# Kernel tuning notes

Hardware: AMD Instinct MI355X
Metric: run time of the kernel (lower is better)

The kernel has to match this reference:

```python
import jax, jax.numpy as jnp
import numpy as np

EPS = 1e-12

def _l2norm(x):
    return x * jax.lax.rsqrt(jnp.maximum(jnp.sum(x * x, -1, keepdims=True), EPS))

def _reverse_seq(x, lens):
    # per-row reversal of the first `lens[b]` steps (tf.reverse_sequence semantics)
    T = x.shape[1]
    ar = jnp.arange(T)[None, :]
    idx = jnp.where(ar < lens[:, None], lens[:, None] - 1 - ar, ar)
    return jnp.take_along_axis(x, idx[:, :, None], axis=1)

def _lstm(x, lens, Wx, Wh, b):
    # x: [B,T,D]; outputs zeroed past lens, state frozen past lens (dynamic_rnn)
    B, T, _ = x.shape
    H = Wh.shape[0]
    xW = jnp.einsum('btd,dh->bth', x, Wx) + b  # [B,T,4H]
    def step(carry, inp):
        h, c = carry
        xw_t, t = inp
        gates = xw_t + h @ Wh
        i, f, g, o = jnp.split(gates, 4, axis=-1)
        c_new = jax.nn.sigmoid(f) * c + jax.nn.sigmoid(i) * jnp.tanh(g)
        h_new = jax.nn.sigmoid(o) * jnp.tanh(c_new)
        valid = (t < lens)[:, None]
        return (jnp.where(valid, h_new, h), jnp.where(valid, c_new, c)), jnp.where(valid, h_new, 0.0)
    z = jnp.zeros((B, H), x.dtype)
    _, outs = jax.lax.scan(step, (z, z), (xW.transpose(1, 0, 2), jnp.arange(T)))
    return outs.transpose(1, 0, 2)

def _bilstm(x, lens, Wx_f, Wh_f, b_f, Wx_b, Wh_b, b_b):
    fwd = _lstm(x, lens, Wx_f, Wh_f, b_f)
    bwd = _reverse_seq(_lstm(_reverse_seq(x, lens), lens, Wx_b, Wh_b, b_b), lens)
    return jnp.concatenate([fwd, bwd], -1)  # [B,T,2R]

def setup_inputs() -> dict:
    B, T, CTX, D, R, HA, TD = 4096, 80, 10, 300, 200, 100, 256
    V, NTOK, NTY, PL = 100000, 250, 113, 3
    ks = jax.random.split(jax.random.key(0), 16)
    f32 = jnp.float32
    return {
        'input_data': jax.random.randint(ks[0], (B, T), 0, V, jnp.int32),
        'entMentIndex': jax.random.randint(ks[1], (B, 5), 0, B * T, jnp.int32),
        'entCtxLeftIndex': jax.random.randint(ks[2], (B, CTX), 0, B * T, jnp.int32),
        'entCtxRightIndex': jax.random.randint(ks[3], (B, CTX), 0, B * T, jnp.int32),
        'entMentLent': jnp.full((B, 1), 5.0, f32),
        'ctxLeftLent': jnp.full((B, 1), float(CTX), f32),
        'ctxRightLent': jnp.full((B, 1), float(CTX), f32),
        'type_path': jax.random.randint(ks[4], (NTY, PL), 0, NTOK, jnp.int32),
        'word_embed': jax.random.normal(ks[5], (V, D), f32) * 0.1,
        'h_m': jax.random.normal(ks[6], (D, HA), f32) * 0.01,
        'h1': jax.random.normal(ks[7], (2 * R, HA), f32) * 0.01,
        'h2': jax.random.normal(ks[8], (HA, 1), f32) * 0.01,
        'Wx_f': jax.random.normal(ks[9], (D, 4 * R), f32) * 0.05,
        'Wh_f': jax.random.normal(ks[10], (R, 4 * R), f32) * 0.05,
        'b_f': jnp.zeros((4 * R,), f32),
        'Wx_b': jax.random.normal(ks[11], (D, 4 * R), f32) * 0.05,
        'Wh_b': jax.random.normal(ks[12], (R, 4 * R), f32) * 0.05,
        'b_b': jnp.zeros((4 * R,), f32),
        'dense_W': jax.random.normal(ks[13], (D + 2 * R, TD), f32) * 0.05,
        'dense_b': jnp.zeros((TD,), f32),
        'type_tok': jax.random.normal(ks[14], (NTOK, TD), f32) * 0.01,
    }

def reference(input_data, entMentIndex, entCtxLeftIndex, entCtxRightIndex,
              entMentLent, ctxLeftLent, ctxRightLent, type_path, word_embed,
              h_m, h1, h2, Wx_f, Wh_f, b_f, Wx_b, Wh_b, b_b,
              dense_W, dense_b, type_tok):
    D = word_embed.shape[1]
    # flattened sentence embeddings with zero padding row at the end
    flat = jnp.concatenate(
        [jnp.take(word_embed, input_data.reshape(-1), axis=0),
         jnp.zeros((1, D), word_embed.dtype)], 0)
    # mention feature: mean of mention word vectors
    f1 = jnp.take(flat, entMentIndex, axis=0).sum(1) / entMentLent  # [B,D]
    # context features via shared BiLSTM
    left = jnp.take(flat, entCtxLeftIndex, axis=0)
    right = jnp.take(flat, entCtxRightIndex, axis=0)
    f2 = _bilstm(left, ctxLeftLent[:, 0].astype(jnp.int32), Wx_f, Wh_f, b_f, Wx_b, Wh_b, b_b)
    f3 = _bilstm(right, ctxRightLent[:, 0].astype(jnp.int32), Wx_f, Wh_f, b_f, Wx_b, Wh_b, b_b)
    ctx = jnp.concatenate([f2, f3], 1)  # [B, 2*CTX, 2R]
    # attention pooling (non-BBN branch uses relu)
    att = jax.nn.relu(jnp.einsum('btr,rh->bth', ctx, h1) + (f1 @ h_m)[:, None, :])
    w = jax.nn.softmax((att @ h2)[:, :, 0], axis=-1)  # [B, 2*CTX]
    ctx_feat = jnp.einsum('btr,bt->br', ctx, w)
    feat = jnp.concatenate([f1, ctx_feat], 1)  # [B, D+2R]
    ent = _l2norm(jax.nn.relu(feat @ dense_W + dense_b))  # [B, TD]
    # type-path embeddings: sum token embeddings along path, l2-normalize
    type_pad = jnp.concatenate([type_tok, jnp.zeros((1, type_tok.shape[1]), type_tok.dtype)], 0)
    type_norm = _l2norm(jnp.take(type_pad, type_path, axis=0).sum(1))  # [NTY, TD]
    return ent @ type_norm.T  # [B, NTY]
```

## Files before the change

kernel.cpp:

```cpp
#include <hip/hip_runtime.h>
#include <hip/hip_bf16.h>

constexpr int B    = 4096;
constexpr int T    = 80;
constexpr int CTXN = 10;
constexpr int D    = 300;
constexpr int R    = 200;
constexpr int HA   = 100;
constexpr int TD   = 256;
constexpr int NTY  = 113;
constexpr int PL   = 3;
constexpr int NTOK = 250;
constexpr int CTX2 = 20;
constexpr int R2   = 400;
constexpr int FEAT = 700;

constexpr int XSB  = 320;
constexpr int KH   = 256;
constexpr int KW   = 576;
constexpr int NB   = 832;
constexpr int CTXS = 448;
constexpr int F1S  = 320;
constexpr int FBS  = 704;
constexpr int FMS  = 128;
constexpr int MX   = 2 * B * CTXN;

typedef __attribute__((ext_vector_type(8))) short bf16x8;
typedef __attribute__((ext_vector_type(4))) float f32x4;

__device__ __forceinline__ ushort f2bf(float f) {
    union { float f; uint32_t u; } x{f};
    uint32_t r = x.u + 0x7fff + ((x.u >> 16) & 1);
    return (ushort)(r >> 16);
}
__device__ __forceinline__ float bf2f(ushort u) {
    union { uint32_t u; float f; } x{(uint32_t)u << 16};
    return x.f;
}

#define GLD_LDS(g, l) __builtin_amdgcn_global_load_lds( \
    (const __attribute__((address_space(1))) void*)(g), \
    (__attribute__((address_space(3))) void*)(l), 16, 0, 0)

constexpr int NWC = 2 * NB * KW;
__global__ void k_prepw3(const float* __restrict__ Wx_f, const float* __restrict__ Wh_f,
                         const float* __restrict__ bf_, const float* __restrict__ Wx_b,
                         const float* __restrict__ Wh_b, const float* __restrict__ bb_,
                         ushort* __restrict__ Wcat, float* __restrict__ biasb) {
    int gid = blockIdx.x * blockDim.x + threadIdx.x;
    if (gid < NWC) {
        int k = gid % KW;
        int q = gid / KW;
        int np = q % NB, dir = q / NB;
        int rb = np >> 6, g = (np >> 4) & 3, ri = np & 15;
        int r = rb * 16 + ri, col = g * 200 + r;
        float v = 0.f;
        if (r < R) {
            if (k < KH) {
                if (k < R) v = (dir ? Wh_b : Wh_f)[(size_t)k * 800 + col];
            } else {
                int kx = k - KH;
                if (kx < D) v = (dir ? Wx_b : Wx_f)[(size_t)kx * 800 + col];
            }
        }
        Wcat[gid] = f2bf(v);
    } else if (gid < NWC + 2 * NB) {
        int t = gid - NWC;
        int np = t % NB, dirb = t / NB;
        int rb = np >> 6, g = (np >> 4) & 3, ri = np & 15;
        int r = rb * 16 + ri, col = g * 200 + r;
        biasb[t] = (r < R) ? (dirb ? bb_ : bf_)[col] : 0.f;
    }
}

__global__ void k_preph1(const float* __restrict__ h1, ushort* __restrict__ h1t) {
    int gid = blockIdx.x * blockDim.x + threadIdx.x;
    if (gid >= FMS * CTXS) return;
    int k = gid % CTXS, n = gid / CTXS;
    float v = (n < HA && k < R2) ? h1[(size_t)k * HA + n] : 0.f;
    h1t[gid] = f2bf(v);
}
__global__ void k_prephm(const float* __restrict__ h_m, ushort* __restrict__ h_mt) {
    int gid = blockIdx.x * blockDim.x + threadIdx.x;
    if (gid >= FMS * F1S) return;
    int k = gid % F1S, n = gid / F1S;
    float v = (n < HA && k < D) ? h_m[(size_t)k * HA + n] : 0.f;
    h_mt[gid] = f2bf(v);
}
__global__ void k_prepdw(const float* __restrict__ dW, ushort* __restrict__ dWt) {
    int gid = blockIdx.x * blockDim.x + threadIdx.x;
    if (gid >= TD * FBS) return;
    int k = gid % FBS, n = gid / FBS;
    float v = (k < FEAT) ? dW[(size_t)k * TD + n] : 0.f;
    dWt[gid] = f2bf(v);
}

__global__ void k_gatherb(const int* __restrict__ idxL, const int* __restrict__ idxR,
                          const int* __restrict__ input_data,
                          const float* __restrict__ we,
                          ushort* __restrict__ xb) {
    int row = blockIdx.x * 4 + (threadIdx.x >> 6);
    int lane = threadIdx.x & 63;
    if (row >= MX) return;
    int side = row / (B * CTXN);
    int bt = row % (B * CTXN);
    int idx = (side ? idxR : idxL)[bt];
    int w = (idx >= 0 && idx < B * T) ? input_data[idx] : -1;
    ushort* dst = xb + (size_t)row * XSB;
    if (lane < XSB / 8) {
        int e0 = lane * 8;
        ushort tmp[8];
        #pragma unroll
        for (int j = 0; j < 8; ++j) {
            int e = e0 + j;
            float f = (w >= 0 && e < D) ? we[(size_t)w * D + e] : 0.f;
            tmp[j] = f2bf(f);
        }
        *reinterpret_cast<bf16x8*>(dst + e0) = *reinterpret_cast<bf16x8*>(tmp);
    }
}

__global__ void k_f1(const int* __restrict__ ment_idx,
                     const float* __restrict__ ment_lent,
                     const int* __restrict__ input_data,
                     const float* __restrict__ we,
                     ushort* __restrict__ featb, ushort* __restrict__ f1b) {
    int b = blockIdx.x;
    __shared__ int wrow[5];
    if (threadIdx.x < 5) {
        int idx = ment_idx[b * 5 + threadIdx.x];
        wrow[threadIdx.x] = (idx >= 0 && idx < B * T) ? input_data[idx] : -1;
    }
    __syncthreads();
    float inv = 1.0f / ment_lent[b];
    for (int d = threadIdx.x; d < F1S; d += blockDim.x) {
        float s = 0.f;
        if (d < D) {
            #pragma unroll
            for (int j = 0; j < 5; ++j) {
                int w = wrow[j];
                if (w >= 0) s += we[(size_t)w * D + d];
            }
            s *= inv;
        }
        ushort u = f2bf(s);
        if (d < D) featb[(size_t)b * FBS + d] = u;
        f1b[(size_t)b * F1S + d] = u;
    }
}

template<int MODE>
__global__ __launch_bounds__(256) void k_mfma(
    const ushort* __restrict__ A, int lda,
    const ushort* __restrict__ Bt, int ldb,
    float* __restrict__ C, int ldc, int K,
    const float* __restrict__ aux) {
    __shared__ __align__(16) ushort As[128 * 64];
    __shared__ __align__(16) ushort Bs[64 * 64];
    int tid = threadIdx.x, wave = tid >> 6, lane = tid & 63;
    int m0 = blockIdx.y * 128, n0 = blockIdx.x * 64;
    int wr = wave >> 1, wc = wave & 1;
    f32x4 acc[4][2] = {};

    for (int k0 = 0; k0 < K; k0 += 64) {
        #pragma unroll
        for (int p = 0; p < 4; ++p) {
            int chunk = p * 4 + wave;
            int row = chunk * 8 + (lane >> 3);
            int ss = (lane & 7) ^ (row & 7);
            GLD_LDS(A + (size_t)(m0 + row) * lda + k0 + ss * 8, As + chunk * 512);
        }
        #pragma unroll
        for (int p = 0; p < 2; ++p) {
            int chunk = p * 4 + wave;
            int row = chunk * 8 + (lane >> 3);
            int ss = (lane & 7) ^ (row & 7);
            GLD_LDS(Bt + (size_t)(n0 + row) * ldb + k0 + ss * 8, Bs + chunk * 512);
        }
        __syncthreads();
        #pragma unroll
        for (int kk = 0; kk < 2; ++kk) {
            bf16x8 a[4], bf[2];
            #pragma unroll
            for (int m = 0; m < 4; ++m) {
                int r = wr * 64 + m * 16 + (lane & 15);
                int ss = (kk * 4 + (lane >> 4)) ^ (r & 7);
                a[m] = *(const bf16x8*)&As[r * 64 + ss * 8];
            }
            #pragma unroll
            for (int n = 0; n < 2; ++n) {
                int r = wc * 32 + n * 16 + (lane & 15);
                int ss = (kk * 4 + (lane >> 4)) ^ (r & 7);
                bf[n] = *(const bf16x8*)&Bs[r * 64 + ss * 8];
            }
            #pragma unroll
            for (int m = 0; m < 4; ++m)
                #pragma unroll
                for (int n = 0; n < 2; ++n)
                    acc[m][n] = __builtin_amdgcn_mfma_f32_16x16x32_bf16(a[m], bf[n], acc[m][n], 0, 0, 0);
        }
        __syncthreads();
    }
    #pragma unroll
    for (int m = 0; m < 4; ++m) {
        #pragma unroll
        for (int n = 0; n < 2; ++n) {
            int c = n0 + wc * 32 + n * 16 + (lane & 15);
            #pragma unroll
            for (int j = 0; j < 4; ++j) {
                int rr = m0 + wr * 64 + m * 16 + (lane >> 4) * 4 + j;
                float v = acc[m][n][j];
                if (MODE == 1) v = fmaxf(v + aux[c], 0.f);
                C[(size_t)rr * ldc + c] = v;
            }
        }
    }
}

__global__ __launch_bounds__(512, 1) void k_lstm(
    const ushort* __restrict__ xb,
    const ushort* __restrict__ Wcat,
    const float* __restrict__ biasb,
    const float* __restrict__ lentL, const float* __restrict__ lentR,
    ushort* __restrict__ ctxb) {
    __shared__ __align__(16) ushort hS[64 * 256];
    __shared__ __align__(16) ushort xS[64 * 320];
    __shared__ __align__(16) ushort wS[8][2][2048];
    __shared__ int lenS[64];
    __shared__ int xrowS[CTXN][64];

    const int tid = threadIdx.x, wave = tid >> 6, lane = tid & 63;
    const int z = blockIdx.x >> 6, rg = blockIdx.x & 63;
    const int side = z >> 1, dir = z & 1;
    const int b0 = rg * 64;
    const ushort* Wd = Wcat + (size_t)dir * NB * KW;
    const int rl = lane & 15, ch = lane >> 4;

    if (tid < 64) {
        int b = b0 + tid;
        int len = (int)((side ? lentR : lentL)[b]);
        len = min(max(len, 0), CTXN);
        lenS[tid] = len;
        for (int s = 0; s < CTXN; ++s) {
            int tt = dir ? ((s < len) ? (len - 1 - s) : s) : s;
            xrowS[s][tid] = (side * (B * CTXN) + b * CTXN + tt) * XSB;
        }
    }
    {
        uint4 zz{0, 0, 0, 0};
        for (int i = tid; i < 64 * 256 / 8; i += 512)
            reinterpret_cast<uint4*>(hS)[i] = zz;
    }
    {
        bf16x8 zz{};
        int ng = dir ? 31 : 25;
        int coff = dir ? R : 0;
        for (int i = tid; i < 640 * ng; i += 512) {
            int bt = i / ng, gix = i - bt * ng;
            int row = bt / CTXN, t = bt - row * CTXN;
            *reinterpret_cast<bf16x8*>(
                ctxb + ((size_t)(b0 + row) * CTX2 + side * CTXN + t) * CTXS + coff + gix * 8) = zz;
        }
    }

    const int nrb = (wave + 8 < 13) ? 2 : 1;
    float bias_[2][4];
    #pragma unroll
    for (int g = 0; g < 4; ++g) {
        bias_[0][g] = biasb[dir * NB + wave * 64 + g * 16 + rl];
        bias_[1][g] = (nrb > 1) ? biasb[dir * NB + (wave + 8) * 64 + g * 16 + rl] : 0.f;
    }
    float cst[2][16];
    #pragma unroll
    for (int i = 0; i < 2; ++i)
        #pragma unroll
        for (int j = 0; j < 16; ++j) cst[i][j] = 0.f;

    __syncthreads();

    #pragma unroll
    for (int i = 0; i < 5; ++i) {
        int chunk = wave * 5 + i;
        int p = chunk * 64 + lane;
        int row = p / 40, c8s = p - row * 40;
        int c8 = c8s ^ (row & 7);
        GLD_LDS(xb + xrowS[0][row] + c8 * 8, xS + chunk * 512);
    }
    __syncthreads();

    float hnew[2][16];

    for (int s = 0; s < CTXN; ++s) {
        const int kstart = (s == 0) ? KH : 0;
        #pragma unroll
        for (int rbi = 0; rbi < 2; ++rbi) {
            if (rbi < nrb) {
                const int rb = rbi ? (wave + 8) : wave;
                const ushort* wb = Wd + (size_t)rb * 64 * KW;
                const int nit = (KW - kstart) >> 5;
                f32x4 acc[4][4];
                #pragma unroll
                for (int m = 0; m < 4; ++m)
                    #pragma unroll
                    for (int g = 0; g < 4; ++g) acc[m][g] = f32x4{0.f, 0.f, 0.f, 0.f};

                #pragma unroll
                for (int i = 0; i < 4; ++i) {
                    int p = i * 64 + lane;
                    int n = p >> 2, c8s = p & 3;
                    int c8 = c8s ^ ((n >> 1) & 3);
                    GLD_LDS(wb + (size_t)n * KW + kstart + c8 * 8, &wS[wave][0][0] + i * 512);
                }
                for (int t = 0; t < nit; ++t) {
                    int k0 = kstart + t * 32;
                    if (t + 1 < nit) {
                        int k1 = k0 + 32;
                        ushort* dst = &wS[wave][(t + 1) & 1][0];
                        #pragma unroll
                        for (int i = 0; i < 4; ++i) {
                            int p = i * 64 + lane;
                            int n = p >> 2, c8s = p & 3;
                            int c8 = c8s ^ ((n >> 1) & 3);
                            GLD_LDS(wb + (size_t)n * KW + k1 + c8 * 8, dst + i * 512);
                        }
                        asm volatile("s_waitcnt vmcnt(4)" ::: "memory");
                    } else {
                        asm volatile("s_waitcnt vmcnt(0)" ::: "memory");
                    }
                    const ushort* abase; int astr, kof;
                    if (k0 < KH) { abase = hS; astr = 256; kof = k0 >> 3; }
                    else         { abase = xS; astr = 320; kof = (k0 - KH) >> 3; }
                    bf16x8 af[4];
                    #pragma unroll
                    for (int m = 0; m < 4; ++m) {
                        int row = m * 16 + rl;
                        int g = (kof + ch) ^ (row & 7);
                        af[m] = *reinterpret_cast<const bf16x8*>(&abase[row * astr + g * 8]);
                    }
                    const ushort* wbuf = &wS[wave][t & 1][0];
                    bf16x8 bfr[4];
                    #pragma unroll
                    for (int g4 = 0; g4 < 4; ++g4) {
                        int col = g4 * 16 + rl;
                        int c8 = ch ^ ((rl >> 1) & 3);
                        bfr[g4] = *reinterpret_cast<const bf16x8*>(&wbuf[col * 32 + c8 * 8]);
                    }
                    #pragma unroll
                    for (int m = 0; m < 4; ++m)
                        #pragma unroll
                        for (int g4 = 0; g4 < 4; ++g4)
                            acc[m][g4] = __builtin_amdgcn_mfma_f32_16x16x32_bf16(
                                af[m], bfr[g4], acc[m][g4], 0, 0, 0);
                }
                #pragma unroll
                for (int m = 0; m < 4; ++m) {
                    #pragma unroll
                    for (int j = 0; j < 4; ++j) {
                        int row = m * 16 + ch * 4 + j;
                        float gi = acc[m][0][j] + bias_[rbi][0];
                        float gf = acc[m][1][j] + bias_[rbi][1];
                        float gg = acc[m][2][j] + bias_[rbi][2];
                        float go = acc[m][3][j] + bias_[rbi][3];
                        float si = 1.f / (1.f + __expf(-gi));
                        float sf = 1.f / (1.f + __expf(-gf));
                        float so = 1.f / (1.f + __expf(-go));
                        float cn = sf * cst[rbi][m * 4 + j] + si * tanhf(gg);
                        float hn = so * tanhf(cn);
                        if (s < lenS[row]) cst[rbi][m * 4 + j] = cn;
                        hnew[rbi][m * 4 + j] = hn;
                    }
                }
            }
        }
        __syncthreads();
        #pragma unroll
        for (int rbi = 0; rbi < 2; ++rbi) {
            if (rbi < nrb) {
                const int rb = rbi ? (wave + 8) : wave;
                const int r = rb * 16 + rl;
                if (r < R) {
                    #pragma unroll
                    for (int m = 0; m < 4; ++m) {
                        #pragma unroll
                        for (int j = 0; j < 4; ++j) {
                            int row = m * 16 + ch * 4 + j;
                            int len = lenS[row];
                            if (s < len) {
                                ushort hv = f2bf(hnew[rbi][m * 4 + j]);
                                hS[row * 256 + (((r >> 3) ^ (row & 7)) << 3) + (r & 7)] = hv;
                                int tpos = dir ? (len - 1 - s) : s;
                                ctxb[((size_t)(b0 + row) * CTX2 + side * CTXN + tpos) * CTXS
                                     + dir * R + r] = hv;
                            }
                        }
                    }
                }
            }
        }
        if (s + 1 < CTXN) {
            #pragma unroll
            for (int i = 0; i < 5; ++i) {
                int chunk = wave * 5 + i;
                int p = chunk * 64 + lane;
                int row = p / 40, c8s = p - row * 40;
                int c8 = c8s ^ (row & 7);
                GLD_LDS(xb + xrowS[s + 1][row] + c8 * 8, xS + chunk * 512);
            }
        }
        __syncthreads();
    }
}

__global__ __launch_bounds__(256) void k_attsc(
    const ushort* __restrict__ ctxb, const ushort* __restrict__ h1t,
    const float* __restrict__ fm, const float* __restrict__ h2,
    float* __restrict__ scores) {
    __shared__ __align__(16) ushort As[128 * 64];
    __shared__ __align__(16) ushort Bs[128 * 64];
    __shared__ float sred[128][2];
    __shared__ float h2s[128];
    int tid = threadIdx.x, wave = tid >> 6, lane = tid & 63;
    int m0 = blockIdx.x * 128;
    if (tid < 128) h2s[tid] = (tid < HA) ? h2[tid] : 0.f;
    int wr = wave >> 1, wc = wave & 1;
    f32x4 acc[4][4] = {};

    for (int k0 = 0; k0 < CTXS; k0 += 64) {
        #pragma unroll
        for (int p = 0; p < 4; ++p) {
            int chunk = p * 4 + wave;
            int row = chunk * 8 + (lane >> 3);
            int ss = (lane & 7) ^ (row & 7);
            GLD_LDS(ctxb + (size_t)(m0 + row) * CTXS + k0 + ss * 8, As + chunk * 512);
        }
        #pragma unroll
        for (int p = 0; p < 4; ++p) {
            int chunk = p * 4 + wave;
            int row = chunk * 8 + (lane >> 3);
            int ss = (lane & 7) ^ (row & 7);
            GLD_LDS(h1t + (size_t)row * CTXS + k0 + ss * 8, Bs + chunk * 512);
        }
        __syncthreads();
        #pragma unroll
        for (int kk = 0; kk < 2; ++kk) {
            bf16x8 a[4], bf[4];
            #pragma unroll
            for (int m = 0; m < 4; ++m) {
                int r = wr * 64 + m * 16 + (lane & 15);
                int ss = (kk * 4 + (lane >> 4)) ^ (r & 7);
                a[m] = *(const bf16x8*)&As[r * 64 + ss * 8];
            }
            #pragma unroll
            for (int n = 0; n < 4; ++n) {
                int r = wc * 64 + n * 16 + (lane & 15);
                int ss = (kk * 4 + (lane >> 4)) ^ (r & 7);
                bf[n] = *(const bf16x8*)&Bs[r * 64 + ss * 8];
            }
            #pragma unroll
            for (int m = 0; m < 4; ++m)
                #pragma unroll
                for (int n = 0; n < 4; ++n)
                    acc[m][n] = __builtin_amdgcn_mfma_f32_16x16x32_bf16(a[m], bf[n], acc[m][n], 0, 0, 0);
        }
        __syncthreads();
    }
    #pragma unroll
    for (int m = 0; m < 4; ++m) {
        #pragma unroll
        for (int j = 0; j < 4; ++j) {
            int rl = wr * 64 + m * 16 + (lane >> 4) * 4 + j;
            int brow = (m0 + rl) / CTX2;
            float v = 0.f;
            #pragma unroll
            for (int n = 0; n < 4; ++n) {
                int c = wc * 64 + n * 16 + (lane & 15);
                float a = acc[m][n][j] + fm[(size_t)brow * FMS + c];
                v += fmaxf(a, 0.f) * h2s[c];
            }
            #pragma unroll
            for (int o = 1; o < 16; o <<= 1) v += __shfl_xor(v, o, 64);
            if ((lane & 15) == 0) sred[rl][wc] = v;
        }
    }
    __syncthreads();
    if (tid < 128) scores[m0 + tid] = sred[tid][0] + sred[tid][1];
}

__global__ void k_att2(const float* __restrict__ scores,
                       const ushort* __restrict__ ctxb,
                       ushort* __restrict__ featb) {
    int b = blockIdx.x;
    float sc[CTX2];
    #pragma unroll
    for (int t = 0; t < CTX2; ++t) sc[t] = scores[b * CTX2 + t];
    float mx = -1e30f;
    #pragma unroll
    for (int t = 0; t < CTX2; ++t) mx = fmaxf(mx, sc[t]);
    float w[CTX2], sum = 0.f;
    #pragma unroll
    for (int t = 0; t < CTX2; ++t) { w[t] = __expf(sc[t] - mx); sum += w[t]; }
    float inv = 1.f / sum;
    for (int col = threadIdx.x; col < R2; col += 256) {
        float acc = 0.f;
        #pragma unroll
        for (int t = 0; t < CTX2; ++t)
            acc += w[t] * bf2f(ctxb[((size_t)b * CTX2 + t) * CTXS + col]);
        featb[(size_t)b * FBS + D + col] = f2bf(acc * inv);
    }
    if (threadIdx.x < FBS - FEAT)
        featb[(size_t)b * FBS + FEAT + threadIdx.x] = 0;
}

__device__ __forceinline__ float blk_sum_256(float v, float* red) {
    #pragma unroll
    for (int o = 32; o > 0; o >>= 1) v += __shfl_down(v, o, 64);
    int lane = threadIdx.x & 63, wid = threadIdx.x >> 6;
    if (lane == 0) red[wid] = v;
    __syncthreads();
    float t = red[0] + red[1] + red[2] + red[3];
    __syncthreads();
    return t;
}

__global__ void k_l2norm(float* __restrict__ x, int ncol) {
    int row = blockIdx.x;
    float* p = x + (size_t)row * ncol;
    __shared__ float red[4];
    float ss = 0.f;
    for (int c = threadIdx.x; c < ncol; c += 256) { float v = p[c]; ss += v * v; }
    float tot = blk_sum_256(ss, red);
    float scale = 1.f / sqrtf(fmaxf(tot, 1e-12f));
    for (int c = threadIdx.x; c < ncol; c += 256) p[c] *= scale;
}

__global__ void k_typenorm(const int* __restrict__ type_path,
                           const float* __restrict__ type_tok,
                           float* __restrict__ tnorm) {
    int y = blockIdx.x;
    int c = threadIdx.x;
    __shared__ float red[4];
    float s = 0.f;
    #pragma unroll
    for (int j = 0; j < PL; ++j) {
        int tk = type_path[y * PL + j];
        if (tk >= 0 && tk < NTOK) s += type_tok[(size_t)tk * TD + c];
    }
    float tot = blk_sum_256(s * s, red);
    float scale = 1.f / sqrtf(fmaxf(tot, 1e-12f));
    tnorm[(size_t)y * TD + c] = s * scale;
}

__global__ void k_final(const float* __restrict__ ent,
                        const float* __restrict__ tnorm,
                        float* __restrict__ out) {
    int b = blockIdx.x;
    __shared__ float es[TD];
    for (int c = threadIdx.x; c < TD; c += blockDim.x) es[c] = ent[(size_t)b * TD + c];
    __syncthreads();
    for (int y = threadIdx.x; y < NTY; y += blockDim.x) {
        const float* tn = tnorm + (size_t)y * TD;
        float acc = 0.f;
        #pragma unroll 4
        for (int k = 0; k < TD; ++k) acc += es[k] * tn[k];
        out[(size_t)b * NTY + y] = acc;
    }
}

static inline char* wsalloc(char*& p, size_t bytes) {
    char* r = p;
    p += (bytes + 255) & ~(size_t)255;
    return r;
}

extern "C" void kernel_launch(void* const* d_in, const int* in_sizes, int n_in,
                              void* d_out, int out_size, void* d_ws, size_t ws_size,
                              hipStream_t stream) {
    const int*   input_data       = (const int*)d_in[0];
    const int*   entMentIndex     = (const int*)d_in[1];
    const int*   entCtxLeftIndex  = (const int*)d_in[2];
    const int*   entCtxRightIndex = (const int*)d_in[3];
    const float* entMentLent      = (const float*)d_in[4];
    const float* ctxLeftLent      = (const float*)d_in[5];
    const float* ctxRightLent     = (const float*)d_in[6];
    const int*   type_path        = (const int*)d_in[7];
    const float* word_embed       = (const float*)d_in[8];
    const float* h_m              = (const float*)d_in[9];
    const float* h1               = (const float*)d_in[10];
    const float* h2               = (const float*)d_in[11];
    const float* Wx_f             = (const float*)d_in[12];
    const float* Wh_f             = (const float*)d_in[13];
    const float* b_f              = (const float*)d_in[14];
    const float* Wx_b             = (const float*)d_in[15];
    const float* Wh_b             = (const float*)d_in[16];
    const float* b_b              = (const float*)d_in[17];
    const float* dense_W          = (const float*)d_in[18];
    const float* dense_b          = (const float*)d_in[19];
    const float* type_tok         = (const float*)d_in[20];
    float* out = (float*)d_out;

    char* p = (char*)d_ws;
    ushort* xb    = (ushort*)wsalloc(p, (size_t)MX * XSB * 2);
    ushort* ctxb  = (ushort*)wsalloc(p, (size_t)B * CTX2 * CTXS * 2);
    ushort* featb = (ushort*)wsalloc(p, (size_t)B * FBS * 2);
    ushort* f1b   = (ushort*)wsalloc(p, (size_t)B * F1S * 2);
    float*  fm    = (float*) wsalloc(p, (size_t)B * FMS * 4);
    float*  scores= (float*) wsalloc(p, (size_t)MX * 4);
    float*  ent   = (float*) wsalloc(p, (size_t)B * TD * 4);
    float*  tnorm = (float*) wsalloc(p, (size_t)NTY * TD * 4);
    ushort* Wcat  = (ushort*)wsalloc(p, (size_t)2 * NB * KW * 2);
    float*  biasb = (float*) wsalloc(p, (size_t)2 * NB * 4);
    ushort* h1t   = (ushort*)wsalloc(p, (size_t)FMS * CTXS * 2);
    ushort* h_mt  = (ushort*)wsalloc(p, (size_t)FMS * F1S * 2);
    ushort* dWt   = (ushort*)wsalloc(p, (size_t)TD * FBS * 2);

    {
        int tot = NWC + 2 * NB;
        k_prepw3<<<(tot + 255) / 256, 256, 0, stream>>>(Wx_f, Wh_f, b_f, Wx_b, Wh_b, b_b,
                                                        Wcat, biasb);
    }
    k_preph1<<<(FMS * CTXS + 255) / 256, 256, 0, stream>>>(h1, h1t);
    k_prephm<<<(FMS * F1S + 255) / 256, 256, 0, stream>>>(h_m, h_mt);
    k_prepdw<<<(TD * FBS + 255) / 256, 256, 0, stream>>>(dense_W, dWt);

    k_gatherb<<<(MX + 3) / 4, 256, 0, stream>>>(entCtxLeftIndex, entCtxRightIndex,
                                                input_data, word_embed, xb);
    k_f1<<<B, 256, 0, stream>>>(entMentIndex, entMentLent, input_data, word_embed, featb, f1b);

    k_mfma<3><<<dim3(FMS / 64, B / 128), 256, 0, stream>>>(f1b, F1S, h_mt, F1S, fm, FMS, F1S, nullptr);

    k_lstm<<<256, 512, 0, stream>>>(xb, Wcat, biasb, ctxLeftLent, ctxRightLent, ctxb);

    k_attsc<<<MX / 128, 256, 0, stream>>>(ctxb, h1t, fm, h2, scores);
    k_att2<<<B, 256, 0, stream>>>(scores, ctxb, featb);

    k_mfma<1><<<dim3(TD / 64, B / 128), 256, 0, stream>>>(featb, FBS, dWt, FBS,
                                                          ent, TD, FBS, dense_b);
    k_l2norm<<<B, 256, 0, stream>>>(ent, TD);
    k_typenorm<<<NTY, TD, 0, stream>>>(type_path, type_tok, tnorm);
    k_final<<<B, 128, 0, stream>>>(ent, tnorm, out);
}
```

Baseline: 630.0 us.

## Pipeline LSTM weight tiles across row blocks and prefetch next-step inputs to registers

The LSTM kernel now streams weight tiles as one continuous double-buffered sequence across both row blocks, instead of draining and restarting the pipeline per block. It loads the next timestep's input rows into registers a few tiles early and writes them to LDS after the barrier. Barriers become explicit waitcnt plus s_barrier, and blocks are remapped so each XCD handles a single direction, which should improve L2 reuse of that direction's weights. Output stores use nontemporal hints. The hand-set vmcnt values must match the number of loads actually in flight, so miscounting risks races and adds fragility.

```diff
diff --git a/kernel.cpp b/kernel.cpp
--- a/kernel.cpp
+++ b/kernel.cpp
@@ -116,7 +116,8 @@
             float f = (w >= 0 && e < D) ? we[(size_t)w * D + e] : 0.f;
             tmp[j] = f2bf(f);
         }
-        *reinterpret_cast<bf16x8*>(dst + e0) = *reinterpret_cast<bf16x8*>(tmp);
+        __builtin_nontemporal_store(*reinterpret_cast<bf16x8*>(tmp),
+                                    reinterpret_cast<bf16x8*>(dst + e0));
     }
 }
 
@@ -230,8 +231,12 @@
     __shared__ int xrowS[CTXN][64];
 
     const int tid = threadIdx.x, wave = tid >> 6, lane = tid & 63;
-    const int z = blockIdx.x >> 6, rg = blockIdx.x & 63;
-    const int side = z >> 1, dir = z & 1;
+    const int bid = blockIdx.x;
+    const int xcd = bid & 7;
+    const int dir = xcd >> 2;
+    const int idx = (xcd & 3) * 32 + (bid >> 3);
+    const int side = idx >> 6, rg = idx & 63;
+    const int z = side * 2 + dir;
     const int b0 = rg * 64;
     const ushort* Wd = Wcat + (size_t)dir * NB * KW;
     const int rl = lane & 15, ch = lane >> 4;
@@ -258,8 +263,8 @@
         for (int i = tid; i < 640 * ng; i += 512) {
             int bt = i / ng, gix = i - bt * ng;
             int row = bt / CTXN, t = bt - row * CTXN;
-            *reinterpret_cast<bf16x8*>(
-                ctxb + ((size_t)(b0 + row) * CTX2 + side * CTXN + t) * CTXS + coff + gix * 8) = zz;
+            __builtin_nontemporal_store(zz, reinterpret_cast<bf16x8*>(
+                ctxb + ((size_t)(b0 + row) * CTX2 + side * CTXN + t) * CTXS + coff + gix * 8));
         }
     }
 
@@ -292,41 +297,68 @@
 
     for (int s = 0; s < CTXN; ++s) {
         const int kstart = (s == 0) ? KH : 0;
+        const int nit = (KW - kstart) >> 5;
+        const int ntile = nrb * nit;
+        const bool xpf = (s + 1 < CTXN);
+        uint4 xreg[5];
+        int xout = 0;
+
+        {
+            const ushort* wb = Wd + (size_t)wave * 64 * KW;
+            #pragma unroll
+            for (int i = 0; i < 4; ++i) {
+                int p = i * 64 + lane;
+                int n = p >> 2, c8s = p & 3;
+                int c8 = c8s ^ ((n >> 1) & 3);
+                GLD_LDS(wb + (size_t)n * KW + kstart + c8 * 8, &wS[wave][0][0] + i * 512);
+            }
+        }
+
+        int gtile = 0;
         #pragma unroll
         for (int rbi = 0; rbi < 2; ++rbi) {
             if (rbi < nrb) {
-                const int rb = rbi ? (wave + 8) : wave;
-                const ushort* wb = Wd + (size_t)rb * 64 * KW;
-                const int nit = (KW - kstart) >> 5;
+                const int rb = wave + rbi * 8;
                 f32x4 acc[4][4];
                 #pragma unroll
                 for (int m = 0; m < 4; ++m)
                     #pragma unroll
                     for (int g = 0; g < 4; ++g) acc[m][g] = f32x4{0.f, 0.f, 0.f, 0.f};
 
-                #pragma unroll
-                for (int i = 0; i < 4; ++i) {
-                    int p = i * 64 + lane;
-                    int n = p >> 2, c8s = p & 3;
-                    int c8 = c8s ^ ((n >> 1) & 3);
-                    GLD_LDS(wb + (size_t)n * KW + kstart + c8 * 8, &wS[wave][0][0] + i * 512);
-                }
-                for (int t = 0; t < nit; ++t) {
-                    int k0 = kstart + t * 32;
-                    if (t + 1 < nit) {
-                        int k1 = k0 + 32;
-                        ushort* dst = &wS[wave][(t + 1) & 1][0];
+                for (int t = 0; t < nit; ++t, ++gtile) {
+                    const bool hasnext = (gtile + 1 < ntile);
+                    if (hasnext) {
+                        int nrbi = (t + 1 < nit) ? rbi : rbi + 1;
+                        int ntt  = (t + 1 < nit) ? t + 1 : 0;
+                        const ushort* wb = Wd + (size_t)(wave + nrbi * 8) * 64 * KW;
+                        ushort* dst = &wS[wave][(gtile + 1) & 1][0];
                         #pragma unroll
                         for (int i = 0; i < 4; ++i) {
                             int p = i * 64 + lane;
                             int n = p >> 2, c8s = p & 3;
                             int c8 = c8s ^ ((n >> 1) & 3);
-                            GLD_LDS(wb + (size_t)n * KW + k1 + c8 * 8, dst + i * 512);
+                            GLD_LDS(wb + (size_t)n * KW + kstart + ntt * 32 + c8 * 8, dst + i * 512);
                         }
-                        asm volatile("s_waitcnt vmcnt(4)" ::: "memory");
+                    }
+                    if (xpf && gtile == ntile - 5) {
+                        #pragma unroll
+                        for (int i = 0; i < 5; ++i) {
+                            int p = (wave * 5 + i) * 64 + lane;
+                            int row = p / 40, c8s = p - row * 40;
+                            int c8 = c8s ^ (row & 7);
+                            xreg[i] = *reinterpret_cast<const uint4*>(xb + xrowS[s + 1][row] + c8 * 8);
+                        }
+                        xout = 1;
+                    }
+                    if (hasnext) {
+                        if (xout) asm volatile("s_waitcnt vmcnt(9)" ::: "memory");
+                        else      asm volatile("s_waitcnt vmcnt(4)" ::: "memory");
                     } else {
-                        asm volatile("s_waitcnt vmcnt(0)" ::: "memory");
+                        if (xout) asm volatile("s_waitcnt vmcnt(5)" ::: "memory");
+                        else      asm volatile("s_waitcnt vmcnt(0)" ::: "memory");
                     }
+
+                    const int k0 = kstart + t * 32;
                     const ushort* abase; int astr, kof;
                     if (k0 < KH) { abase = hS; astr = 256; kof = k0 >> 3; }
                     else         { abase = xS; astr = 320; kof = (k0 - KH) >> 3; }
@@ -337,7 +369,7 @@
                         int g = (kof + ch) ^ (row & 7);
                         af[m] = *reinterpret_cast<const bf16x8*>(&abase[row * astr + g * 8]);
                     }
-                    const ushort* wbuf = &wS[wave][t & 1][0];
+                    const ushort* wbuf = &wS[wave][gtile & 1][0];
                     bf16x8 bfr[4];
                     #pragma unroll
                     for (int g4 = 0; g4 < 4; ++g4) {
@@ -372,11 +404,13 @@
                 }
             }
         }
-        __syncthreads();
+        asm volatile("s_waitcnt lgkmcnt(0)" ::: "memory");
+        __builtin_amdgcn_s_barrier();
+
         #pragma unroll
         for (int rbi = 0; rbi < 2; ++rbi) {
             if (rbi < nrb) {
-                const int rb = rbi ? (wave + 8) : wave;
+                const int rb = wave + rbi * 8;
                 const int r = rb * 16 + rl;
                 if (r < R) {
                     #pragma unroll
@@ -389,25 +423,25 @@
                                 ushort hv = f2bf(hnew[rbi][m * 4 + j]);
                                 hS[row * 256 + (((r >> 3) ^ (row & 7)) << 3) + (r & 7)] = hv;
                                 int tpos = dir ? (len - 1 - s) : s;
-                                ctxb[((size_t)(b0 + row) * CTX2 + side * CTXN + tpos) * CTXS
-                                     + dir * R + r] = hv;
+                                __builtin_nontemporal_store(hv,
+                                    ctxb + ((size_t)(b0 + row) * CTX2 + side * CTXN + tpos) * CTXS
+                                         + dir * R + r);
                             }
                         }
                     }
                 }
             }
         }
-        if (s + 1 < CTXN) {
+        if (xpf) {
             #pragma unroll
             for (int i = 0; i < 5; ++i) {
-                int chunk = wave * 5 + i;
-                int p = chunk * 64 + lane;
-                int row = p / 40, c8s = p - row * 40;
-                int c8 = c8s ^ (row & 7);
-                GLD_LDS(xb + xrowS[s + 1][row] + c8 * 8, xS + chunk * 512);
-            }
-        }
-        __syncthreads();
+                int p = (wave * 5 + i) * 64 + lane;
+                *reinterpret_cast<bf16x8*>(&xS[p * 8]) =
+                    *reinterpret_cast<const bf16x8*>(&xreg[i]);
+            }
+        }
+        asm volatile("s_waitcnt vmcnt(0) lgkmcnt(0)" ::: "memory");
+        __builtin_amdgcn_s_barrier();
     }
 }
 
```

New measurement: 708.4 us. 12.4% more time.

## Stage LSTM outputs in LDS and write ctx rows as coalesced 16-byte stores

Applied to the files above, without the earlier changes.

The upfront zero-fill of the ctx buffer is removed. Each step now writes h values (zeros for padded steps) into a per-wave LDS staging buffer, and after a barrier the block copies them to global memory as bf16x8 vector stores. This replaces scattered 2-byte global stores and the separate zeroing pass. It also swaps __syncthreads for explicit waitcnt+s_barrier and adds a third barrier per step, with a vmcnt(0) wait that may stall on global stores. Correctness relies on wS being an existing buffer that is free at this point, and padding columns beyond 2R are no longer zeroed, which assumes later kernels ignore them.

```diff
diff --git a/kernel.cpp b/kernel.cpp
--- a/kernel.cpp
+++ b/kernel.cpp
@@ -250,17 +250,6 @@
         uint4 zz{0, 0, 0, 0};
         for (int i = tid; i < 64 * 256 / 8; i += 512)
             reinterpret_cast<uint4*>(hS)[i] = zz;
-    }
-    {
-        bf16x8 zz{};
-        int ng = dir ? 31 : 25;
-        int coff = dir ? R : 0;
-        for (int i = tid; i < 640 * ng; i += 512) {
-            int bt = i / ng, gix = i - bt * ng;
-            int row = bt / CTXN, t = bt - row * CTXN;
-            *reinterpret_cast<bf16x8*>(
-                ctxb + ((size_t)(b0 + row) * CTX2 + side * CTXN + t) * CTXS + coff + gix * 8) = zz;
-        }
     }
 
     const int nrb = (wave + 8 < 13) ? 2 : 1;
@@ -372,27 +361,24 @@
                 }
             }
         }
-        __syncthreads();
+        asm volatile("s_waitcnt lgkmcnt(0)" ::: "memory");
+        __builtin_amdgcn_s_barrier();
+
         #pragma unroll
         for (int rbi = 0; rbi < 2; ++rbi) {
             if (rbi < nrb) {
-                const int rb = rbi ? (wave + 8) : wave;
+                const int rb = wave + rbi * 8;
                 const int r = rb * 16 + rl;
-                if (r < R) {
+                #pragma unroll
+                for (int m = 0; m < 4; ++m) {
                     #pragma unroll
-                    for (int m = 0; m < 4; ++m) {
-                        #pragma unroll
-                        for (int j = 0; j < 4; ++j) {
-                            int row = m * 16 + ch * 4 + j;
-                            int len = lenS[row];
-                            if (s < len) {
-                                ushort hv = f2bf(hnew[rbi][m * 4 + j]);
-                                hS[row * 256 + (((r >> 3) ^ (row & 7)) << 3) + (r & 7)] = hv;
-                                int tpos = dir ? (len - 1 - s) : s;
-                                ctxb[((size_t)(b0 + row) * CTX2 + side * CTXN + tpos) * CTXS
-                                     + dir * R + r] = hv;
-                            }
-                        }
+                    for (int j = 0; j < 4; ++j) {
+                        int row = m * 16 + ch * 4 + j;
+                        bool live = (s < lenS[row]);
+                        ushort hv = f2bf(live ? hnew[rbi][m * 4 + j] : 0.f);
+                        wS[wave][1][row * 32 + rbi * 16 + rl] = hv;
+                        if (live && r < R)
+                            hS[row * 256 + (((r >> 3) ^ (row & 7)) << 3) + (r & 7)] = hv;
                     }
                 }
             }
@@ -407,7 +393,22 @@
                 GLD_LDS(xb + xrowS[s + 1][row] + c8 * 8, xS + chunk * 512);
             }
         }
-        __syncthreads();
+        asm volatile("s_waitcnt lgkmcnt(0)" ::: "memory");
+        __builtin_amdgcn_s_barrier();
+
+        for (int i = tid; i < 64 * 25; i += 512) {
+            int row = i / 25, g = i - row * 25;
+            int len = lenS[row];
+            int tp = (s < len) ? (dir ? (len - 1 - s) : s) : s;
+            int rb2 = g >> 1;
+            int w = rb2 & 7, rbi = rb2 >> 3;
+            int off = (g & 1) * 8;
+            bf16x8 v = *reinterpret_cast<const bf16x8*>(&wS[w][1][row * 32 + rbi * 16 + off]);
+            *reinterpret_cast<bf16x8*>(
+                ctxb + ((size_t)(b0 + row) * CTX2 + side * CTXN + tp) * CTXS + dir * R + g * 8) = v;
+        }
+        asm volatile("s_waitcnt vmcnt(0) lgkmcnt(0)" ::: "memory");
+        __builtin_amdgcn_s_barrier();
     }
 }
 
```

After: 594.6 us. 5.6% less time.
